# Performance work log

Measured on AMD Instinct MI355X. Metric: run time of the kernel, lower is better.

The kernel has to match this reference:

```python
import jax, jax.numpy as jnp
import numpy as np

B, H, WD = 4, 1440, 1440      # batch, BEV grid (sparse_shape)
N, C, NB = 200000, 32, 3      # active voxels, channels, num basic blocks
EPS = 1e-3                    # BatchNorm1d eps in the module


def setup_inputs() -> dict:
    key = jax.random.key(0)
    ks = jax.random.split(key, 10)
    feats = jax.random.normal(ks[0], (N, C), jnp.float32)
    coords_b = jax.random.randint(ks[1], (N,), 0, B, dtype=jnp.int32)
    coords_y = jax.random.randint(ks[2], (N,), 0, H, dtype=jnp.int32)
    coords_x = jax.random.randint(ks[3], (N,), 0, WD, dtype=jnp.int32)
    # [block, conv(2), tap(3x3=9), Cin, Cout]; fan-in scaled init
    Wk = jax.random.normal(ks[4], (NB, 2, 9, C, C), jnp.float32) / np.sqrt(9 * C)
    bias = 0.01 * jax.random.normal(ks[5], (NB, 2, C), jnp.float32)
    gamma = 1.0 + 0.1 * jax.random.normal(ks[6], (NB, 2, C), jnp.float32)
    beta = 0.1 * jax.random.normal(ks[7], (NB, 2, C), jnp.float32)
    mean = 0.1 * jax.random.normal(ks[8], (NB, 2, C), jnp.float32)
    var = jax.random.uniform(ks[9], (NB, 2, C), jnp.float32, 0.5, 1.5)
    return dict(feats=feats, Wk=Wk, bias=bias, gamma=gamma, beta=beta,
                mean=mean, var=var, coords_b=coords_b, coords_y=coords_y,
                coords_x=coords_x)


def _build_rulebook(coords_b, coords_y, coords_x):
    # Dense hash: grid cell -> voxel row id (-1 if empty). Shared by all
    # submanifold convs in the stage (same indice_key in the original).
    idx_map = jnp.full((B, H, WD), -1, jnp.int32)
    idx_map = idx_map.at[coords_b, coords_y, coords_x].set(
        jnp.arange(N, dtype=jnp.int32))
    offs = jnp.array([(dy, dx) for dy in (-1, 0, 1) for dx in (-1, 0, 1)],
                     jnp.int32)                      # [9,2]
    ny = coords_y[None, :] + offs[:, 0:1]            # [9,N]
    nx = coords_x[None, :] + offs[:, 1:2]
    inb = (ny >= 0) & (ny < H) & (nx >= 0) & (nx < WD)
    nyc = jnp.clip(ny, 0, H - 1)
    nxc = jnp.clip(nx, 0, WD - 1)
    nidx = idx_map[jnp.broadcast_to(coords_b[None, :], (9, N)), nyc, nxc]
    mask = inb & (nidx >= 0)
    nidx = jnp.where(mask, nidx, 0)                  # safe gather index
    return nidx, mask[..., None].astype(jnp.float32)


def reference(feats, Wk, bias, gamma, beta, mean, var,
              coords_b, coords_y, coords_x):
    nidx, maskf = _build_rulebook(coords_b, coords_y, coords_x)

    def subm(x, w, b):
        # gather-GEMM-scatter submanifold 3x3 conv on active sites only
        g = x[nidx] * maskf                          # [9,N,Cin]
        return jnp.einsum('knc,kco->no', g, w) + b   # [N,Cout]

    def bn(x, g_, b_, m_, v_):
        return (x - m_) * jax.lax.rsqrt(v_ + EPS) * g_ + b_

    h = feats
    for i in range(NB):  # SparseBasicBlock stack (fixed small layer count)
        identity = h
        o = jax.nn.relu(bn(subm(h, Wk[i, 0], bias[i, 0]),
                           gamma[i, 0], beta[i, 0], mean[i, 0], var[i, 0]))
        o = bn(subm(o, Wk[i, 1], bias[i, 1]),
               gamma[i, 1], beta[i, 1], mean[i, 1], var[i, 1])
        h = jax.nn.relu(o + identity)
    return h
```

## Files before the change

kernel.cpp:

```cpp
#include <hip/hip_runtime.h>

#define NB_ 3
#define CB 4
#define CH 1440
#define CW 1440
#define NC 32
#define EPSV 1e-3f

#define HBITS 19
#define HSIZE (1u << HBITS)
#define HMASK (HSIZE - 1)

typedef __attribute__((ext_vector_type(8))) short bf16x8;
typedef __attribute__((ext_vector_type(16))) float f32x16;

union U16 { uint4 u; bf16x8 v; };

__device__ __forceinline__ unsigned pk2(float a, float b) {
    unsigned ua = __float_as_uint(a), ub = __float_as_uint(b);
    ua += 0x7fffu + ((ua >> 16) & 1u);
    ub += 0x7fffu + ((ub >> 16) & 1u);
    return (ua >> 16) | (ub & 0xffff0000u);
}
__device__ __forceinline__ unsigned short f2b(float a) {
    unsigned u = __float_as_uint(a);
    u += 0x7fffu + ((u >> 16) & 1u);
    return (unsigned short)(u >> 16);
}
__device__ __forceinline__ float b2f(unsigned short s) {
    return __uint_as_float(((unsigned)s) << 16);
}

__device__ __forceinline__ unsigned hash_of(unsigned key) {
    return (key * 2654435761u) >> (32 - HBITS);
}

__global__ __launch_bounds__(256) void k_hinsert(
    const int* __restrict__ cb, const int* __restrict__ cy, const int* __restrict__ cx,
    unsigned long long* __restrict__ tab, int n)
{
    int i = blockIdx.x * blockDim.x + threadIdx.x;
    if (i >= n) return;
    unsigned key = ((unsigned)cb[i] * CH + (unsigned)cy[i]) * CW + (unsigned)cx[i];
    unsigned long long pk = (((unsigned long long)(key + 1)) << 32) | (unsigned)i;
    unsigned h = hash_of(key);
    for (;;) {
        unsigned long long old = atomicCAS(&tab[h], 0ull, pk);
        if (old == 0ull) break;
        if ((unsigned)(old >> 32) == key + 1) { atomicMax(&tab[h], pk); break; }
        h = (h + 1) & HMASK;
    }
}

__device__ __forceinline__ int hquery(const unsigned long long* __restrict__ tab,
                                      unsigned key)
{
    unsigned h = hash_of(key);
    for (;;) {
        unsigned long long v = tab[h];
        if (v == 0ull) return -1;
        if ((unsigned)(v >> 32) == key + 1) return (int)(v & 0xffffffffu);
        h = (h + 1) & HMASK;
    }
}

__global__ __launch_bounds__(256) void k_prep(
    const int* __restrict__ cb, const int* __restrict__ cy, const int* __restrict__ cx,
    const unsigned long long* __restrict__ tab, int* __restrict__ roff,
    const float* __restrict__ feats, unsigned short* __restrict__ xbf,
    const float* __restrict__ Wk, uint4* __restrict__ Bfg,
    unsigned short* __restrict__ z0, unsigned short* __restrict__ z1,
    unsigned short* __restrict__ z2, int n)
{
    int RB = (n + 255) >> 8;
    int CVT = ((n * NC / 8) + 255) >> 8;
    int bx = blockIdx.x;

    if (bx < RB) {
        int i = bx * 256 + threadIdx.x;
        if (i >= n) return;
        int b = cb[i], y = cy[i], x = cx[i];
        unsigned key = ((unsigned)b * CH + (unsigned)y) * CW + (unsigned)x;
        roff[4 * n + i] = hquery(tab, key) * 64;
        #pragma unroll
        for (int k = 0; k < 9; ++k) {
            if (k == 4) continue;
            int dy = k / 3 - 1, dx = k % 3 - 1;
            int ny = y + dy, nx = x + dx;
            int nb = -1;
            if (ny >= 0 && ny < CH && nx >= 0 && nx < CW)
                nb = hquery(tab, key + dy * CW + dx);
            roff[k * n + i] = (nb >= 0) ? nb * 64 : -1;
        }
    } else if (bx < RB + CVT) {
        int i = ((bx - RB) * 256 + threadIdx.x) * 8;
        if (i + 8 <= n * NC) {
            float4 a0 = *(const float4*)(feats + i);
            float4 a1 = *(const float4*)(feats + i + 4);
            uint4 r;
            r.x = pk2(a0.x, a0.y); r.y = pk2(a0.z, a0.w);
            r.z = pk2(a1.x, a1.y); r.w = pk2(a1.z, a1.w);
            *(uint4*)(xbf + i) = r;
        }
    } else {
        int wb = bx - RB - CVT;
        if (wb == 0 && threadIdx.x < 12) {
            uint4 z = make_uint4(0, 0, 0, 0);
            int tt = threadIdx.x;
            if (tt < 4)       ((uint4*)z0)[tt] = z;
            else if (tt < 8)  ((uint4*)z1)[tt - 4] = z;
            else              ((uint4*)z2)[tt - 8] = z;
        }
        int t = wb * 256 + threadIdx.x;
        if (t >= 6 * 9 * 2 * 64) return;
        int l = t & 63, h = (t >> 6) & 1;
        int rest = t >> 7;
        int k = rest % 9, layer = rest / 9;
        int o = l & 31;
        int c0 = h * 16 + 8 * (l >> 5);
        const float* wp = Wk + (size_t)layer * 9216 + k * 1024 + o;
        uint4 r;
        r.x = pk2(wp[(c0 + 0) * 32], wp[(c0 + 1) * 32]);
        r.y = pk2(wp[(c0 + 2) * 32], wp[(c0 + 3) * 32]);
        r.z = pk2(wp[(c0 + 4) * 32], wp[(c0 + 5) * 32]);
        r.w = pk2(wp[(c0 + 6) * 32], wp[(c0 + 7) * 32]);
        Bfg[t] = r;
    }
}

template<bool ADD_ID, bool F32OUT>
__global__ __launch_bounds__(256, 6) void k_conv(
    const unsigned short* __restrict__ in,
    const unsigned short* __restrict__ idn,
    void* __restrict__ outv,
    const uint4* __restrict__ Bf,
    const float* __restrict__ bias,
    const float* __restrict__ gamma, const float* __restrict__ beta,
    const float* __restrict__ mean, const float* __restrict__ var,
    const int* __restrict__ roff, int n)
{
    int l = threadIdx.x & 63, wv = threadIdx.x >> 6;
    int q = l & 31, h5 = l >> 5;

    int ntile = (n + 31) >> 5;
    int tile = blockIdx.x * 4 + wv;
    if (tile >= ntile) return;

    float sc = gamma[q] * rsqrtf(var[q] + EPSV);
    float sh = (bias[q] - mean[q]) * sc + beta[q];

    const int zoff = n * 64;
    const char* inB = (const char*)in;

    int p0 = tile << 5;
    int pr = p0 + q;
    bool rowok = pr < n;
    int prc = rowok ? pr : n - 1;

    int rk[9];
    #pragma unroll
    for (int k = 0; k < 9; ++k) rk[k] = roff[(size_t)k * n + prc];

    f32x16 acc = {0.f,0.f,0.f,0.f,0.f,0.f,0.f,0.f,0.f,0.f,0.f,0.f,0.f,0.f,0.f,0.f};

    #pragma unroll
    for (int g = 0; g < 3; ++g) {
        bool act[3];
        U16 a0[3], a1[3];
        #pragma unroll
        for (int j = 0; j < 3; ++j) {
            int k = g * 3 + j;
            act[j] = __any(rk[k] >= 0);
            if (act[j]) {
                int off = (rowok && rk[k] >= 0) ? rk[k] : zoff;
                const char* ap = inB + off + h5 * 16;
                a0[j].u = *(const uint4*)(ap);
                a1[j].u = *(const uint4*)(ap + 32);
            }
        }
        #pragma unroll
        for (int j = 0; j < 3; ++j) {
            int k = g * 3 + j;
            if (act[j]) {
                U16 b0, b1;
                b0.u = Bf[(k * 2 + 0) * 64 + l];
                b1.u = Bf[(k * 2 + 1) * 64 + l];
                acc = __builtin_amdgcn_mfma_f32_32x32x16_bf16(a0[j].v, b0.v, acc, 0, 0, 0);
                acc = __builtin_amdgcn_mfma_f32_32x32x16_bf16(a1[j].v, b1.v, acc, 0, 0, 0);
            }
        }
    }

    #pragma unroll
    for (int r = 0; r < 16; ++r) {
        int p = p0 + (r & 3) + 8 * (r >> 2) + 4 * h5;
        if (p < n) {
            float y = acc[r] * sc + sh;
            if (ADD_ID) y += b2f(idn[(size_t)p * 32 + q]);
            y = fmaxf(y, 0.f);
            if (F32OUT) ((float*)outv)[(size_t)p * 32 + q] = y;
            else ((unsigned short*)outv)[(size_t)p * 32 + q] = f2b(y);
        }
    }
}

extern "C" void kernel_launch(void* const* d_in, const int* in_sizes, int n_in,
                              void* d_out, int out_size, void* d_ws, size_t ws_size,
                              hipStream_t stream)
{
    const float* feats = (const float*)d_in[0];
    const float* Wk    = (const float*)d_in[1];
    const float* bias  = (const float*)d_in[2];
    const float* gamma = (const float*)d_in[3];
    const float* beta  = (const float*)d_in[4];
    const float* mean  = (const float*)d_in[5];
    const float* var   = (const float*)d_in[6];
    const int* cb = (const int*)d_in[7];
    const int* cy = (const int*)d_in[8];
    const int* cx = (const int*)d_in[9];
    float* out = (float*)d_out;
    int n = in_sizes[0] / NC;

    char* ws = (char*)d_ws;
    unsigned long long* tab  = (unsigned long long*)(ws + 0);
    int*            roff     = (int*)(ws + 4194304);
    uint4*          Bfg      = (uint4*)(ws + 11394304);
    unsigned short* xbf      = (unsigned short*)(ws + 11504896);
    unsigned short* tmpbf    = (unsigned short*)(ws + 24304960);
    unsigned short* hb       = (unsigned short*)(ws + 37105024);

    hipMemsetAsync(tab, 0, (size_t)HSIZE * 8, stream);

    int RB  = (n + 255) / 256;
    int CVT = ((n * NC / 8) + 255) / 256;
    k_hinsert<<<RB, 256, 0, stream>>>(cb, cy, cx, tab, n);
    k_prep<<<RB + CVT + 27, 256, 0, stream>>>(
        cb, cy, cx, tab, roff, feats, xbf, Wk, Bfg,
        xbf + (size_t)n * 32, tmpbf + (size_t)n * 32, hb + (size_t)n * 32, n);

    const int ntile = (n + 31) / 32;
    const int G = (ntile + 3) / 4;
    const int BSZ = 9 * 2 * 64;

    k_conv<false, false><<<G, 256, 0, stream>>>(xbf, nullptr, tmpbf,
        Bfg + 0 * BSZ, bias + 0,  gamma + 0,  beta + 0,  mean + 0,  var + 0,  roff, n);
    k_conv<true,  false><<<G, 256, 0, stream>>>(tmpbf, xbf, hb,
        Bfg + 1 * BSZ, bias + 32, gamma + 32, beta + 32, mean + 32, var + 32, roff, n);
    k_conv<false, false><<<G, 256, 0, stream>>>(hb, nullptr, tmpbf,
        Bfg + 2 * BSZ, bias + 64, gamma + 64, beta + 64, mean + 64, var + 64, roff, n);
    k_conv<true,  false><<<G, 256, 0, stream>>>(tmpbf, hb, xbf,
        Bfg + 3 * BSZ, bias + 96, gamma + 96, beta + 96, mean + 96, var + 96, roff, n);
    k_conv<false, false><<<G, 256, 0, stream>>>(xbf, nullptr, tmpbf,
        Bfg + 4 * BSZ, bias + 128, gamma + 128, beta + 128, mean + 128, var + 128, roff, n);
    k_conv<true,  true><<<G, 256, 0, stream>>>(tmpbf, xbf, out,
        Bfg + 5 * BSZ, bias + 160, gamma + 160, beta + 160, mean + 160, var + 160, roff, n);
}
```

Baseline: 141.5 us.

## Replace open-addressing hash table with dense grid index map and validation

Swaps the linear-probing hash table, which needed a 4 MB memset plus atomicCAS inserts, for a dense B*H*W int map. Only the cells of active voxels are cleared, and atomicMax then writes the last voxel index per cell. Neighbour lookups read the map directly and validate each hit by comparing that voxel's packed key, so stale garbage in unset cells is rejected. This removes the memset and the probe chains and adds one extra kernel launch, at the cost of a 33 MB workspace whose random accesses will mostly miss cache.

After: 128.7 us (median of 2 runs). 1.1x faster.

```diff
diff --git a/kernel.cpp b/kernel.cpp
--- a/kernel.cpp
+++ b/kernel.cpp
@@ -7,10 +7,6 @@
 #define NC 32
 #define EPSV 1e-3f
 
-#define HBITS 19
-#define HSIZE (1u << HBITS)
-#define HMASK (HSIZE - 1)
-
 typedef __attribute__((ext_vector_type(8))) short bf16x8;
 typedef __attribute__((ext_vector_type(16))) float f32x16;
 
@@ -31,42 +27,36 @@
     return __uint_as_float(((unsigned)s) << 16);
 }
 
-__device__ __forceinline__ unsigned hash_of(unsigned key) {
-    return (key * 2654435761u) >> (32 - HBITS);
-}
-
-__global__ __launch_bounds__(256) void k_hinsert(
+__global__ __launch_bounds__(256) void k_clear(
     const int* __restrict__ cb, const int* __restrict__ cy, const int* __restrict__ cx,
-    unsigned long long* __restrict__ tab, int n)
+    int* __restrict__ idx_map, unsigned* __restrict__ pkey, int n)
 {
     int i = blockIdx.x * blockDim.x + threadIdx.x;
     if (i >= n) return;
     unsigned key = ((unsigned)cb[i] * CH + (unsigned)cy[i]) * CW + (unsigned)cx[i];
-    unsigned long long pk = (((unsigned long long)(key + 1)) << 32) | (unsigned)i;
-    unsigned h = hash_of(key);
-    for (;;) {
-        unsigned long long old = atomicCAS(&tab[h], 0ull, pk);
-        if (old == 0ull) break;
-        if ((unsigned)(old >> 32) == key + 1) { atomicMax(&tab[h], pk); break; }
-        h = (h + 1) & HMASK;
-    }
-}
-
-__device__ __forceinline__ int hquery(const unsigned long long* __restrict__ tab,
-                                      unsigned key)
-{
-    unsigned h = hash_of(key);
-    for (;;) {
-        unsigned long long v = tab[h];
-        if (v == 0ull) return -1;
-        if ((unsigned)(v >> 32) == key + 1) return (int)(v & 0xffffffffu);
-        h = (h + 1) & HMASK;
-    }
+    pkey[i] = key;
+    idx_map[key] = -1;
+}
+
+__global__ __launch_bounds__(256) void k_build_map(
+    const unsigned* __restrict__ pkey, int* __restrict__ idx_map, int n)
+{
+    int i = blockIdx.x * blockDim.x + threadIdx.x;
+    if (i < n) atomicMax(&idx_map[pkey[i]], i);
+}
+
+__device__ __forceinline__ int vquery(const int* __restrict__ idx_map,
+                                      const unsigned* __restrict__ pkey,
+                                      unsigned cell, int n)
+{
+    int v = idx_map[cell];
+    if (v < 0 || v >= n) return -1;
+    return (pkey[v] == cell) ? v : -1;
 }
 
 __global__ __launch_bounds__(256) void k_prep(
-    const int* __restrict__ cb, const int* __restrict__ cy, const int* __restrict__ cx,
-    const unsigned long long* __restrict__ tab, int* __restrict__ roff,
+    const unsigned* __restrict__ pkey, const int* __restrict__ idx_map,
+    int* __restrict__ roff,
     const float* __restrict__ feats, unsigned short* __restrict__ xbf,
     const float* __restrict__ Wk, uint4* __restrict__ Bfg,
     unsigned short* __restrict__ z0, unsigned short* __restrict__ z1,
@@ -79,17 +69,18 @@
     if (bx < RB) {
         int i = bx * 256 + threadIdx.x;
         if (i >= n) return;
-        int b = cb[i], y = cy[i], x = cx[i];
-        unsigned key = ((unsigned)b * CH + (unsigned)y) * CW + (unsigned)x;
-        roff[4 * n + i] = hquery(tab, key) * 64;
+        unsigned key = pkey[i];
+        unsigned x = key % CW;
+        unsigned y = (key / CW) % CH;
+        roff[4 * n + i] = idx_map[key] * 64;
         #pragma unroll
         for (int k = 0; k < 9; ++k) {
             if (k == 4) continue;
             int dy = k / 3 - 1, dx = k % 3 - 1;
-            int ny = y + dy, nx = x + dx;
+            int ny = (int)y + dy, nx = (int)x + dx;
             int nb = -1;
             if (ny >= 0 && ny < CH && nx >= 0 && nx < CW)
-                nb = hquery(tab, key + dy * CW + dx);
+                nb = vquery(idx_map, pkey, key + dy * CW + dx, n);
             roff[k * n + i] = (nb >= 0) ? nb * 64 : -1;
         }
     } else if (bx < RB + CVT) {
@@ -222,20 +213,20 @@
     int n = in_sizes[0] / NC;
 
     char* ws = (char*)d_ws;
-    unsigned long long* tab  = (unsigned long long*)(ws + 0);
-    int*            roff     = (int*)(ws + 4194304);
-    uint4*          Bfg      = (uint4*)(ws + 11394304);
-    unsigned short* xbf      = (unsigned short*)(ws + 11504896);
-    unsigned short* tmpbf    = (unsigned short*)(ws + 24304960);
-    unsigned short* hb       = (unsigned short*)(ws + 37105024);
-
-    hipMemsetAsync(tab, 0, (size_t)HSIZE * 8, stream);
+    int*            idx_map = (int*)(ws + 0);
+    unsigned*       pkey    = (unsigned*)(ws + 33177600);
+    int*            roff    = (int*)(ws + 33977600);
+    uint4*          Bfg     = (uint4*)(ws + 41177600);
+    unsigned short* xbf     = (unsigned short*)(ws + 41288192);
+    unsigned short* tmpbf   = (unsigned short*)(ws + 54088256);
+    unsigned short* hb      = (unsigned short*)(ws + 66888320);
 
     int RB  = (n + 255) / 256;
     int CVT = ((n * NC / 8) + 255) / 256;
-    k_hinsert<<<RB, 256, 0, stream>>>(cb, cy, cx, tab, n);
+    k_clear<<<RB, 256, 0, stream>>>(cb, cy, cx, idx_map, pkey, n);
+    k_build_map<<<RB, 256, 0, stream>>>(pkey, idx_map, n);
     k_prep<<<RB + CVT + 27, 256, 0, stream>>>(
-        cb, cy, cx, tab, roff, feats, xbf, Wk, Bfg,
+        pkey, idx_map, roff, feats, xbf, Wk, Bfg,
         xbf + (size_t)n * 32, tmpbf + (size_t)n * 32, hb + (size_t)n * 32, n);
 
     const int ntile = (n + 31) / 32;
```
